# Performance work log

Measured on AMD Instinct MI355X. Metric: run time of the kernel, lower is better.

Reference implementation:

```python
import jax, jax.numpy as jnp
import numpy as np
from jax import lax

N = 100000   # n_nodes
E = 600000   # n_edges (no self loops by construction)
D = 128      # hidden_dim
L = 3        # n_hops
K = 5        # tail_k_threshold


def setup_inputs() -> dict:
    key = jax.random.key(0)
    ks = jax.random.split(key, 10)
    x = jax.random.normal(ks[0], (N, D), dtype=jnp.float32)
    src = jax.random.randint(ks[1], (E,), 0, N)
    off = jax.random.randint(ks[2], (E,), 1, N)
    dst = (src + off) % N  # guarantees dst != src (self loops removed in original)
    s = 1.0 / np.sqrt(D)
    def U(k, shape):
        return jax.random.uniform(k, shape, minval=-s, maxval=s, dtype=jnp.float32)
    return {
        "x": x,
        "G1": U(ks[3], (L, D, D)), "G2": U(ks[4], (L, D, D)),
        "B1": U(ks[5], (L, D, D)), "B2": U(ks[6], (L, D, D)),
        "R": U(ks[7], (L, D)),
        "edge_src": src, "edge_dst": dst,
    }


def _lrelu(v):
    return jax.nn.leaky_relu(v, 0.2)


def reference(x, G1, G2, B1, B2, R, edge_src, edge_dst):
    # row degrees of adj (A[src, dst] = 1)
    deg = jax.ops.segment_sum(jnp.ones(E, jnp.float32), edge_src, num_segments=N)
    inv_d = jnp.where(deg > 0, 1.0 / jnp.maximum(deg, 1.0), 0.0)   # left norm D^-1 A
    inv_d1 = 1.0 / (deg + 1.0)                                      # (A+I) left norm
    inv_d2 = 1.0 / (deg + 2.0)                                      # +1 virtual node
    w0, w1, w2 = inv_d[edge_src], inv_d1[edge_src], inv_d2[edge_src]
    head_mask = deg > K

    def spmm(w_edge, h):  # (D^-1 A) @ h via gather-scale-scatter
        return jax.ops.segment_sum(w_edge[:, None] * h[edge_dst], edge_src, num_segments=N)

    def propagate(head):
        h = x
        embs = [h]
        sups = []
        for l in range(L):
            nb = spmm(w0, h)
            ft = lax.stop_gradient(h)
            nbd = lax.stop_gradient(nb)
            gamma = _lrelu(ft @ G1[l].T + nbd @ G2[l].T) + 1.0
            beta = _lrelu(ft @ B1[l].T + nbd @ B2[l].T)
            m = ft + gamma * R[l] + beta - nbd   # missing_info (Relation, ablation=0)
            sups.append(m)
            if head:
                h = spmm(w1, h) + inv_d1[:, None] * h
            else:
                h = spmm(w2, h) + inv_d2[:, None] * h + m * inv_d2[:, None]
            embs.append(h)
        emb = jnp.mean(jnp.stack(embs, 0), 0)
        sup = jnp.mean(jnp.stack(sups, 0), 0)
        return emb, sup

    emb_h, _ = propagate(True)
    emb_t, _ = propagate(False)
    node_emb = jnp.where(head_mask[:, None], emb_h, emb_t)
    return node_emb
```

## Files before the change

### kernel.cpp

```cpp
#include <hip/hip_runtime.h>

#define N_NODES 100000
#define N_EDGES 600000
#define DIM 128
#define SCAN_B 1024
#define NCHUNK 98

typedef __attribute__((ext_vector_type(4))) float f32x4;
typedef __attribute__((ext_vector_type(8))) short bf16x8;
typedef __attribute__((ext_vector_type(4))) unsigned short u16x4;
typedef __attribute__((ext_vector_type(8))) unsigned short u16x8;

__device__ __forceinline__ unsigned short f2bf(float f) {
    union { float f; unsigned u; } cv; cv.f = f;
    unsigned r = (cv.u + 0x7FFFu + ((cv.u >> 16) & 1u)) >> 16;
    return (unsigned short)r;
}
__device__ __forceinline__ float bf2f(unsigned short v) {
    union { unsigned u; float f; } c; c.u = ((unsigned)v) << 16; return c.f;
}


__global__ void k_degree(const int* __restrict__ src, int* __restrict__ degi) {
    int e = blockIdx.x * 256 + threadIdx.x;
    if (e < N_EDGES) atomicAdd(&degi[src[e]], 1);
}

__global__ void k_chunksum(const int* __restrict__ degi, int* __restrict__ bsum) {
    __shared__ int sm[SCAN_B];
    int i = blockIdx.x * SCAN_B + threadIdx.x;
    sm[threadIdx.x] = (i < N_NODES) ? degi[i] : 0;
    __syncthreads();
    for (int s = SCAN_B / 2; s > 0; s >>= 1) {
        if (threadIdx.x < (unsigned)s) sm[threadIdx.x] += sm[threadIdx.x + s];
        __syncthreads();
    }
    if (threadIdx.x == 0) bsum[blockIdx.x] = sm[0];
}

__global__ void k_scanb(int* __restrict__ bsum, int nb) {
    __shared__ int sm[128];
    int t = threadIdx.x;
    int v = (t < nb) ? bsum[t] : 0;
    sm[t] = v; __syncthreads();
    for (int s = 1; s < 128; s <<= 1) {
        int a = (t >= s) ? sm[t - s] : 0;
        __syncthreads();
        sm[t] += a;
        __syncthreads();
    }
    if (t < nb) bsum[t] = sm[t] - v;
}

__global__ void k_rowptr(const int* __restrict__ degi, const int* __restrict__ bsum,
                         int* __restrict__ rowptr, int* __restrict__ cnt,
                         float* __restrict__ inv0, float* __restrict__ inv1,
                         float* __restrict__ inv2) {
    __shared__ int sm[SCAN_B];
    int i = blockIdx.x * SCAN_B + threadIdx.x;
    int v = (i < N_NODES) ? degi[i] : 0;
    sm[threadIdx.x] = v; __syncthreads();
    for (int s = 1; s < SCAN_B; s <<= 1) {
        int a = (threadIdx.x >= (unsigned)s) ? sm[threadIdx.x - s] : 0;
        __syncthreads();
        sm[threadIdx.x] += a;
        __syncthreads();
    }
    if (i < N_NODES) {
        int excl = bsum[blockIdx.x] + sm[threadIdx.x] - v;
        rowptr[i] = excl;
        cnt[i] = excl;
        float d = (float)v;
        inv0[i] = (v > 0) ? 1.0f / d : 0.0f;
        inv1[i] = 1.0f / (d + 1.0f);
        inv2[i] = 1.0f / (d + 2.0f);
    }
}

__global__ void k_fill(const int* __restrict__ src, const int* __restrict__ dst,
                       int* __restrict__ cnt, int* __restrict__ col) {
    int e = blockIdx.x * 256 + threadIdx.x;
    if (e < N_EDGES) {
        int pos = atomicAdd(&cnt[src[e]], 1);
        col[pos] = dst[e];
    }
}

__global__ void k_pack(const float* __restrict__ G1, const float* __restrict__ G2,
                       const float* __restrict__ B1, const float* __restrict__ B2,
                       short* __restrict__ Wp) {
    int idx = blockIdx.x * 256 + threadIdx.x;
    int j = idx & 7, lane = (idx >> 3) & 63, nt = (idx >> 9) & 15, kb = (idx >> 13) & 7, l = idx >> 16;
    int k = kb * 32 + (lane >> 4) * 8 + j;
    int n = nt * 16 + (lane & 15);
    float v;
    if (n < 128) {
        v = (k < 128) ? G1[(l * 128 + n) * 128 + k] : G2[(l * 128 + n) * 128 + (k - 128)];
    } else {
        int n2 = n - 128;
        v = (k < 128) ? B1[(l * 128 + n2) * 128 + k] : B2[(l * 128 + n2) * 128 + (k - 128)];
    }
    Wp[idx] = (short)f2bf(v);
}

__global__ void k_xcast(const float* __restrict__ x, unsigned short* __restrict__ xb) {
    int i = (blockIdx.x * 256 + threadIdx.x) * 4;
    f32x4 v = *(const f32x4*)(x + i);
    unsigned short o0 = f2bf(v[0]), o1 = f2bf(v[1]), o2 = f2bf(v[2]), o3 = f2bf(v[3]);
    unsigned long long pk = (unsigned long long)o0 | ((unsigned long long)o1 << 16)
                          | ((unsigned long long)o2 << 32) | ((unsigned long long)o3 << 48);
    *(unsigned long long*)(xb + i) = pk;
}


template <int NE>
__device__ __forceinline__ void gath_issue(const u16x8* __restrict__ h8,
        int idx, int base, int c, int d, float* acc) {
    u16x8 v[NE];
#pragma unroll
    for (int e = 0; e < NE; ++e) {
        int ce = __shfl(idx, base + e, 64);
        v[e] = h8[(size_t)ce * 16 + c];
    }
#pragma unroll
    for (int e = 0; e < NE; ++e) {
        if (e < d) {
#pragma unroll
            for (int j = 0; j < 8; ++j) acc[j] += bf2f(v[e][j]);
        }
    }
}

__device__ __forceinline__ void gather4(const u16x8* __restrict__ h8,
        const int* __restrict__ col, int start, int d, int lane, float* acc) {
    int c = lane & 15;
    int base = lane & 48;
    int dd = d < 16 ? d : 16;
    int idx = (c < dd) ? col[start + c] : 0;
    int dm = d;
    int tmx = __shfl_xor(dm, 16);
    dm = dm > tmx ? dm : tmx;
    tmx = __shfl_xor(dm, 32);
    dm = dm > tmx ? dm : tmx;
    if (dm <= 8) {
        gath_issue<8>(h8, idx, base, c, d, acc);
    } else {
        gath_issue<16>(h8, idx, base, c, d, acc);
        if (dm > 16) {
            for (int e = 16; e < d; ++e) {
                int c0 = col[start + e];
                u16x8 v = h8[(size_t)c0 * 16 + c];
#pragma unroll
                for (int j = 0; j < 8; ++j) acc[j] += bf2f(v[j]);
            }
        }
    }
}

template <int NE>
__device__ __forceinline__ void gath_issue2(const u16x8* __restrict__ hT,
        const u16x8* __restrict__ hH,
        int idx, int base, int c, int d, int e0, float* accT, float* accH) {
    u16x8 vT[NE], vH[NE];
#pragma unroll
    for (int e = 0; e < NE; ++e) {
        int ce = __shfl(idx, base + e0 + e, 64);
        vT[e] = hT[(size_t)ce * 16 + c];
        vH[e] = hH[(size_t)ce * 16 + c];
    }
#pragma unroll
    for (int e = 0; e < NE; ++e) {
        if (e0 + e < d) {
#pragma unroll
            for (int j = 0; j < 8; ++j) {
                accT[j] += bf2f(vT[e][j]);
                accH[j] += bf2f(vH[e][j]);
            }
        }
    }
}

__device__ __forceinline__ void gather4_dual(const u16x8* __restrict__ hT,
        const u16x8* __restrict__ hH,
        const int* __restrict__ col, int start, int d, int lane,
        float* accT, float* accH) {
    int c = lane & 15;
    int base = lane & 48;
    int dd = d < 16 ? d : 16;
    int idx = (c < dd) ? col[start + c] : 0;
    int dm = d;
    int tmx = __shfl_xor(dm, 16);
    dm = dm > tmx ? dm : tmx;
    tmx = __shfl_xor(dm, 32);
    dm = dm > tmx ? dm : tmx;
    if (dm <= 8) {
        gath_issue2<8>(hT, hH, idx, base, c, d, 0, accT, accH);
    } else {
        gath_issue2<8>(hT, hH, idx, base, c, d, 0, accT, accH);
        gath_issue2<8>(hT, hH, idx, base, c, d, 8, accT, accH);
        if (dm > 16) {
            for (int e = 16; e < d; ++e) {
                int c0 = col[start + e];
                u16x8 vT = hT[(size_t)c0 * 16 + c];
                u16x8 vH = hH[(size_t)c0 * 16 + c];
#pragma unroll
                for (int j = 0; j < 8; ++j) {
                    accT[j] += bf2f(vT[j]);
                    accH[j] += bf2f(vH[j]);
                }
            }
        }
    }
}

__device__ __forceinline__ void tail_gemm(
    int rb,
    unsigned short (*sH)[136], unsigned short (*sS)[136], unsigned short (*sO)[136],
    unsigned short* __restrict__ hb_next,
    const unsigned short* __restrict__ xb, const unsigned short* __restrict__ t1b,
    float* __restrict__ outp,
    const float* __restrict__ Rl, const short* __restrict__ Wp,
    const float* __restrict__ inv0, const float* __restrict__ inv2,
    const int* __restrict__ degi, int last)
{
    int wave = threadIdx.x >> 6, lane = threadIdx.x & 63;
    int q = lane >> 4, m = lane & 15;
    float w0 = inv0[rb + m];
    const short* wl = Wp + lane * 8;

    const f32x4 vz = {0.f, 0.f, 0.f, 0.f};
    f32x4 aA[2] = {vz, vz}, aB[2] = {vz, vz};

#pragma unroll
    for (int kb = 0; kb < 4; ++kb) {
        bf16x8 ah = *(const bf16x8*)&sH[m][kb * 32 + q * 8];
#pragma unroll
        for (int j = 0; j < 2; ++j) {
            bf16x8 b1v = *(const bf16x8*)(wl + (kb * 16 + 2 * wave + j) * 512);
            bf16x8 b2v = *(const bf16x8*)(wl + (kb * 16 + 2 * wave + 8 + j) * 512);
            aA[j] = __builtin_amdgcn_mfma_f32_16x16x32_bf16(ah, b1v, aA[j], 0, 0, 0);
            aB[j] = __builtin_amdgcn_mfma_f32_16x16x32_bf16(ah, b2v, aB[j], 0, 0, 0);
        }
    }
#pragma unroll
    for (int kb = 0; kb < 4; ++kb) {
        u16x8 sv = *(const u16x8*)&sS[m][kb * 32 + q * 8];
        bf16x8 as;
#pragma unroll
        for (int j = 0; j < 8; ++j) as[j] = (short)f2bf(w0 * bf2f(sv[j]));
#pragma unroll
        for (int j = 0; j < 2; ++j) {
            bf16x8 b1v = *(const bf16x8*)(wl + ((kb + 4) * 16 + 2 * wave + j) * 512);
            bf16x8 b2v = *(const bf16x8*)(wl + ((kb + 4) * 16 + 2 * wave + 8 + j) * 512);
            aA[j] = __builtin_amdgcn_mfma_f32_16x16x32_bf16(as, b1v, aA[j], 0, 0, 0);
            aB[j] = __builtin_amdgcn_mfma_f32_16x16x32_bf16(as, b2v, aB[j], 0, 0, 0);
        }
    }

    float Rv[2];
#pragma unroll
    for (int j = 0; j < 2; ++j) Rv[j] = Rl[(2 * wave + j) * 16 + m];

#pragma unroll
    for (int r = 0; r < 4; ++r) {
        int gi = rb + q * 4 + r;
        float wi0 = inv0[gi], wi2 = inv2[gi];
        int dgi = degi[gi];
#pragma unroll
        for (int j = 0; j < 2; ++j) {
            int cc = (2 * wave + j) * 16 + m;
            float z1 = aA[j][r], z2 = aB[j][r];
            float h = bf2f(sH[q * 4 + r][cc]);
            float sva = bf2f(sS[q * 4 + r][cc]);
            float ga = (z1 > 0.f ? z1 : 0.2f * z1) + 1.0f;
            float be = (z2 > 0.f ? z2 : 0.2f * z2);
            float mm = h + ga * Rv[j] + be - wi0 * sva;
            float hn = wi2 * (sva + h + mm);
            if (!last) {
                sO[q * 4 + r][cc] = f2bf(hn);
            } else if (dgi <= 5) {
                float xv = bf2f(xb[(size_t)gi * DIM + cc]);
                float t1 = bf2f(t1b[(size_t)gi * DIM + cc]);
                outp[(size_t)gi * DIM + cc] = 0.25f * (xv + t1 + h + hn);
            }
        }
    }
    if (!last) {
        __syncthreads();
        int g = lane >> 4, c = lane & 15;
        int row = rb + wave * 4 + g;
        ((u16x8*)hb_next)[(size_t)row * 16 + c] = *(u16x8*)&sO[wave * 4 + g][c * 8];
    }
}


__global__ __launch_bounds__(256, 4) void k_fused0(
    const unsigned short* __restrict__ xb, unsigned short* __restrict__ hA,
    unsigned short* __restrict__ tA, float* __restrict__ outp,
    const float* __restrict__ Rl, const short* __restrict__ Wp,
    const float* __restrict__ inv0, const float* __restrict__ inv1,
    const float* __restrict__ inv2,
    const int* __restrict__ rowptr, const int* __restrict__ degi,
    const int* __restrict__ col)
{
    __shared__ __align__(16) unsigned short sH[16][136], sS[16][136], sO[16][136];
    int rb = blockIdx.x * 16;
    int wave = threadIdx.x >> 6, lane = threadIdx.x & 63;
    {
        int g = lane >> 4, c = lane & 15;
        int row = rb + wave * 4 + g;
        int start = rowptr[row], d = degi[row];
        u16x8 hv = ((const u16x8*)xb)[(size_t)row * 16 + c];
        float acc[8] = {0,0,0,0,0,0,0,0};
        gather4((const u16x8*)xb, col, start, d, lane, acc);
        u16x8 so;
#pragma unroll
        for (int j = 0; j < 8; ++j) so[j] = f2bf(acc[j]);
        *(u16x8*)&sS[wave * 4 + g][c * 8] = so;
        *(u16x8*)&sH[wave * 4 + g][c * 8] = hv;
        float w1 = inv1[row];
        u16x8 ho;
#pragma unroll
        for (int j = 0; j < 8; ++j) ho[j] = f2bf(w1 * (acc[j] + bf2f(hv[j])));
        ((u16x8*)hA)[(size_t)row * 16 + c] = ho;
    }
    __syncthreads();
    tail_gemm(rb, sH, sS, sO, tA, xb, tA, outp, Rl, Wp, inv0, inv2, degi, 0);
}

__global__ __launch_bounds__(256, 4) void k_hop(
    const unsigned short* __restrict__ tb, unsigned short* __restrict__ tb_next,
    const unsigned short* __restrict__ hb, unsigned short* __restrict__ hb_next,
    const unsigned short* __restrict__ xb, const unsigned short* __restrict__ t1b,
    const unsigned short* __restrict__ h1b, float* __restrict__ outp,
    const float* __restrict__ Rl, const short* __restrict__ Wp,
    const float* __restrict__ inv0, const float* __restrict__ inv1,
    const float* __restrict__ inv2,
    const int* __restrict__ rowptr, const int* __restrict__ degi,
    const int* __restrict__ col, int last)
{
    __shared__ __align__(16) unsigned short sH[16][136], sS[16][136], sO[16][136];
    int rb = blockIdx.x * 16;
    int wave = threadIdx.x >> 6, lane = threadIdx.x & 63;

    {
        int g = lane >> 4, c = lane & 15;
        int row = rb + wave * 4 + g;
        int start = rowptr[row], d = degi[row];
        u16x8 tv = ((const u16x8*)tb)[(size_t)row * 16 + c];
        u16x8 hv = ((const u16x8*)hb)[(size_t)row * 16 + c];
        float accT[8] = {0,0,0,0,0,0,0,0};
        float accH[8] = {0,0,0,0,0,0,0,0};
        gather4_dual((const u16x8*)tb, (const u16x8*)hb, col, start, d, lane, accT, accH);

        u16x8 so;
#pragma unroll
        for (int j = 0; j < 8; ++j) so[j] = f2bf(accT[j]);
        *(u16x8*)&sS[wave * 4 + g][c * 8] = so;
        *(u16x8*)&sH[wave * 4 + g][c * 8] = tv;

        float w1 = inv1[row];
        if (!last) {
            u16x8 ho;
#pragma unroll
            for (int j = 0; j < 8; ++j) ho[j] = f2bf(w1 * (accH[j] + bf2f(hv[j])));
            ((u16x8*)hb_next)[(size_t)row * 16 + c] = ho;
        } else if (d > 5) {
            u16x8 xv = ((const u16x8*)xb)[(size_t)row * 16 + c];
            u16x8 h1 = ((const u16x8*)h1b)[(size_t)row * 16 + c];
            f32x4 e0, e1;
#pragma unroll
            for (int j = 0; j < 4; ++j) {
                float h2 = bf2f(hv[j]);
                e0[j] = 0.25f * (bf2f(xv[j]) + bf2f(h1[j]) + h2 + w1 * (accH[j] + h2));
            }
#pragma unroll
            for (int j = 0; j < 4; ++j) {
                float h2 = bf2f(hv[4 + j]);
                e1[j] = 0.25f * (bf2f(xv[4 + j]) + bf2f(h1[4 + j]) + h2 + w1 * (accH[4 + j] + h2));
            }
            float* op = outp + (size_t)row * DIM + c * 8;
            *(f32x4*)op = e0;
            *(f32x4*)(op + 4) = e1;
        }
    }
    __syncthreads();

    tail_gemm(rb, sH, sS, sO, tb_next, xb, t1b, outp, Rl, Wp, inv0, inv2, degi, last);
}


extern "C" void kernel_launch(void* const* d_in, const int* in_sizes, int n_in,
                              void* d_out, int out_size, void* d_ws, size_t ws_size,
                              hipStream_t stream) {
    const float* x  = (const float*)d_in[0];
    const float* G1 = (const float*)d_in[1];
    const float* G2 = (const float*)d_in[2];
    const float* B1 = (const float*)d_in[3];
    const float* B2 = (const float*)d_in[4];
    const float* R  = (const float*)d_in[5];
    const int* esrc = (const int*)d_in[6];
    const int* edst = (const int*)d_in[7];
    float* out = (float*)d_out;

    char* base = (char*)d_ws;
    size_t off = 0;
    auto alloc = [&](size_t b) -> void* {
        void* p = base + off;
        off = (off + b + 255) & ~(size_t)255;
        return p;
    };
    int* degi   = (int*)alloc(4 * N_NODES);
    int* rowptr = (int*)alloc(4 * N_NODES);
    int* cnt    = (int*)alloc(4 * N_NODES);
    int* bsum   = (int*)alloc(4 * 256);
    int* col    = (int*)alloc(4 * N_EDGES);
    float* inv0 = (float*)alloc(4 * N_NODES);
    float* inv1 = (float*)alloc(4 * N_NODES);
    float* inv2 = (float*)alloc(4 * N_NODES);
    short* Wp   = (short*)alloc(2 * 3 * 65536);
    unsigned short* xb = (unsigned short*)alloc(2ull * N_NODES * DIM);
    unsigned short* hA = (unsigned short*)alloc(2ull * N_NODES * DIM);
    unsigned short* hB = (unsigned short*)alloc(2ull * N_NODES * DIM);
    unsigned short* tA = (unsigned short*)alloc(2ull * N_NODES * DIM);
    unsigned short* tB = (unsigned short*)alloc(2ull * N_NODES * DIM);

    hipMemsetAsync(degi, 0, 4 * N_NODES, stream);
    k_degree<<<(N_EDGES + 255) / 256, 256, 0, stream>>>(esrc, degi);
    k_chunksum<<<NCHUNK, SCAN_B, 0, stream>>>(degi, bsum);
    k_scanb<<<1, 128, 0, stream>>>(bsum, NCHUNK);
    k_rowptr<<<NCHUNK, SCAN_B, 0, stream>>>(degi, bsum, rowptr, cnt, inv0, inv1, inv2);
    k_fill<<<(N_EDGES + 255) / 256, 256, 0, stream>>>(esrc, edst, cnt, col);
    k_pack<<<768, 256, 0, stream>>>(G1, G2, B1, B2, Wp);
    k_xcast<<<12500, 256, 0, stream>>>(x, xb);

    k_fused0<<<6250, 256, 0, stream>>>(xb, hA, tA, out, R, Wp,
                                       inv0, inv1, inv2, rowptr, degi, col);

    k_hop<<<6250, 256, 0, stream>>>(tA, tB, hA, hB, xb, tA, hA, out,
                                    R + 128, Wp + 65536,
                                    inv0, inv1, inv2, rowptr, degi, col, 0);

    k_hop<<<6250, 256, 0, stream>>>(tB, (unsigned short*)0, hB, (unsigned short*)0,
                                    xb, tA, hA, out,
                                    R + 256, Wp + 131072,
                                    inv0, inv1, inv2, rowptr, degi, col, 1);
}
```

Measured before the change: 397.2 us.

## Interleave tail and head states per node and process 32 rows per block

Replaces the separate tail and head bf16 buffers with one interleaved buffer per hop, so each node's t and h rows sit next to each other (256 halves per node). A neighbour gather then reads one contiguous 512-byte span instead of two scattered 256-byte reads. Blocks now cover 32 rows instead of 16, which reuses the weight fragments across two MFMA row tiles and halves the grid. The cost is more LDS and register use per block, which may lower occupancy.

```diff
diff --git a/kernel.cpp b/kernel.cpp
--- a/kernel.cpp
+++ b/kernel.cpp
@@ -158,15 +158,15 @@
 }
 
 template <int NE>
-__device__ __forceinline__ void gath_issue2(const u16x8* __restrict__ hT,
-        const u16x8* __restrict__ hH,
+__device__ __forceinline__ void gath_issue2c(const u16x8* __restrict__ st8,
         int idx, int base, int c, int d, int e0, float* accT, float* accH) {
     u16x8 vT[NE], vH[NE];
 #pragma unroll
     for (int e = 0; e < NE; ++e) {
         int ce = __shfl(idx, base + e0 + e, 64);
-        vT[e] = hT[(size_t)ce * 16 + c];
-        vH[e] = hH[(size_t)ce * 16 + c];
+        size_t b = (size_t)ce * 32 + c;
+        vT[e] = st8[b];
+        vH[e] = st8[b + 16];
     }
 #pragma unroll
     for (int e = 0; e < NE; ++e) {
@@ -180,8 +180,7 @@
     }
 }
 
-__device__ __forceinline__ void gather4_dual(const u16x8* __restrict__ hT,
-        const u16x8* __restrict__ hH,
+__device__ __forceinline__ void gather4_dualc(const u16x8* __restrict__ st8,
         const int* __restrict__ col, int start, int d, int lane,
         float* accT, float* accH) {
     int c = lane & 15;
@@ -194,15 +193,16 @@
     tmx = __shfl_xor(dm, 32);
     dm = dm > tmx ? dm : tmx;
     if (dm <= 8) {
-        gath_issue2<8>(hT, hH, idx, base, c, d, 0, accT, accH);
+        gath_issue2c<8>(st8, idx, base, c, d, 0, accT, accH);
     } else {
-        gath_issue2<8>(hT, hH, idx, base, c, d, 0, accT, accH);
-        gath_issue2<8>(hT, hH, idx, base, c, d, 8, accT, accH);
+        gath_issue2c<8>(st8, idx, base, c, d, 0, accT, accH);
+        gath_issue2c<8>(st8, idx, base, c, d, 8, accT, accH);
         if (dm > 16) {
             for (int e = 16; e < d; ++e) {
                 int c0 = col[start + e];
-                u16x8 vT = hT[(size_t)c0 * 16 + c];
-                u16x8 vH = hH[(size_t)c0 * 16 + c];
+                size_t b = (size_t)c0 * 32 + c;
+                u16x8 vT = st8[b];
+                u16x8 vH = st8[b + 16];
 #pragma unroll
                 for (int j = 0; j < 8; ++j) {
                     accT[j] += bf2f(vT[j]);
@@ -213,11 +213,12 @@
     }
 }
 
-__device__ __forceinline__ void tail_gemm(
+__device__ __forceinline__ void tail_gemm32(
     int rb,
     unsigned short (*sH)[136], unsigned short (*sS)[136], unsigned short (*sO)[136],
-    unsigned short* __restrict__ hb_next,
-    const unsigned short* __restrict__ xb, const unsigned short* __restrict__ t1b,
+    unsigned short* __restrict__ stn,
+    const unsigned short* __restrict__ st1,
+    const unsigned short* __restrict__ xb,
     float* __restrict__ outp,
     const float* __restrict__ Rl, const short* __restrict__ Wp,
     const float* __restrict__ inv0, const float* __restrict__ inv2,
@@ -225,35 +226,44 @@
 {
     int wave = threadIdx.x >> 6, lane = threadIdx.x & 63;
     int q = lane >> 4, m = lane & 15;
-    float w0 = inv0[rb + m];
+    float w0a = inv0[rb + m], w0b = inv0[rb + 16 + m];
     const short* wl = Wp + lane * 8;
 
     const f32x4 vz = {0.f, 0.f, 0.f, 0.f};
-    f32x4 aA[2] = {vz, vz}, aB[2] = {vz, vz};
+    f32x4 aA[2][2] = {{vz, vz}, {vz, vz}}, aB[2][2] = {{vz, vz}, {vz, vz}};
 
 #pragma unroll
     for (int kb = 0; kb < 4; ++kb) {
-        bf16x8 ah = *(const bf16x8*)&sH[m][kb * 32 + q * 8];
+        bf16x8 ah0 = *(const bf16x8*)&sH[m][kb * 32 + q * 8];
+        bf16x8 ah1 = *(const bf16x8*)&sH[16 + m][kb * 32 + q * 8];
 #pragma unroll
         for (int j = 0; j < 2; ++j) {
             bf16x8 b1v = *(const bf16x8*)(wl + (kb * 16 + 2 * wave + j) * 512);
             bf16x8 b2v = *(const bf16x8*)(wl + (kb * 16 + 2 * wave + 8 + j) * 512);
-            aA[j] = __builtin_amdgcn_mfma_f32_16x16x32_bf16(ah, b1v, aA[j], 0, 0, 0);
-            aB[j] = __builtin_amdgcn_mfma_f32_16x16x32_bf16(ah, b2v, aB[j], 0, 0, 0);
+            aA[0][j] = __builtin_amdgcn_mfma_f32_16x16x32_bf16(ah0, b1v, aA[0][j], 0, 0, 0);
+            aA[1][j] = __builtin_amdgcn_mfma_f32_16x16x32_bf16(ah1, b1v, aA[1][j], 0, 0, 0);
+            aB[0][j] = __builtin_amdgcn_mfma_f32_16x16x32_bf16(ah0, b2v, aB[0][j], 0, 0, 0);
+            aB[1][j] = __builtin_amdgcn_mfma_f32_16x16x32_bf16(ah1, b2v, aB[1][j], 0, 0, 0);
         }
     }
 #pragma unroll
     for (int kb = 0; kb < 4; ++kb) {
-        u16x8 sv = *(const u16x8*)&sS[m][kb * 32 + q * 8];
-        bf16x8 as;
-#pragma unroll
-        for (int j = 0; j < 8; ++j) as[j] = (short)f2bf(w0 * bf2f(sv[j]));
+        u16x8 sv0 = *(const u16x8*)&sS[m][kb * 32 + q * 8];
+        u16x8 sv1 = *(const u16x8*)&sS[16 + m][kb * 32 + q * 8];
+        bf16x8 as0, as1;
+#pragma unroll
+        for (int j = 0; j < 8; ++j) {
+            as0[j] = (short)f2bf(w0a * bf2f(sv0[j]));
+            as1[j] = (short)f2bf(w0b * bf2f(sv1[j]));
+        }
 #pragma unroll
         for (int j = 0; j < 2; ++j) {
             bf16x8 b1v = *(const bf16x8*)(wl + ((kb + 4) * 16 + 2 * wave + j) * 512);
             bf16x8 b2v = *(const bf16x8*)(wl + ((kb + 4) * 16 + 2 * wave + 8 + j) * 512);
-            aA[j] = __builtin_amdgcn_mfma_f32_16x16x32_bf16(as, b1v, aA[j], 0, 0, 0);
-            aB[j] = __builtin_amdgcn_mfma_f32_16x16x32_bf16(as, b2v, aB[j], 0, 0, 0);
+            aA[0][j] = __builtin_amdgcn_mfma_f32_16x16x32_bf16(as0, b1v, aA[0][j], 0, 0, 0);
+            aA[1][j] = __builtin_amdgcn_mfma_f32_16x16x32_bf16(as1, b1v, aA[1][j], 0, 0, 0);
+            aB[0][j] = __builtin_amdgcn_mfma_f32_16x16x32_bf16(as0, b2v, aB[0][j], 0, 0, 0);
+            aB[1][j] = __builtin_amdgcn_mfma_f32_16x16x32_bf16(as1, b2v, aB[1][j], 0, 0, 0);
         }
     }
 
@@ -262,112 +272,123 @@
     for (int j = 0; j < 2; ++j) Rv[j] = Rl[(2 * wave + j) * 16 + m];
 
 #pragma unroll
-    for (int r = 0; r < 4; ++r) {
-        int gi = rb + q * 4 + r;
-        float wi0 = inv0[gi], wi2 = inv2[gi];
-        int dgi = degi[gi];
-#pragma unroll
-        for (int j = 0; j < 2; ++j) {
-            int cc = (2 * wave + j) * 16 + m;
-            float z1 = aA[j][r], z2 = aB[j][r];
-            float h = bf2f(sH[q * 4 + r][cc]);
-            float sva = bf2f(sS[q * 4 + r][cc]);
-            float ga = (z1 > 0.f ? z1 : 0.2f * z1) + 1.0f;
-            float be = (z2 > 0.f ? z2 : 0.2f * z2);
-            float mm = h + ga * Rv[j] + be - wi0 * sva;
-            float hn = wi2 * (sva + h + mm);
-            if (!last) {
-                sO[q * 4 + r][cc] = f2bf(hn);
-            } else if (dgi <= 5) {
-                float xv = bf2f(xb[(size_t)gi * DIM + cc]);
-                float t1 = bf2f(t1b[(size_t)gi * DIM + cc]);
-                outp[(size_t)gi * DIM + cc] = 0.25f * (xv + t1 + h + hn);
+    for (int t = 0; t < 2; ++t) {
+#pragma unroll
+        for (int r = 0; r < 4; ++r) {
+            int rl = t * 16 + q * 4 + r;
+            int gi = rb + rl;
+            float wi0 = inv0[gi], wi2 = inv2[gi];
+            int dgi = degi[gi];
+#pragma unroll
+            for (int j = 0; j < 2; ++j) {
+                int cc = (2 * wave + j) * 16 + m;
+                float z1 = aA[t][j][r], z2 = aB[t][j][r];
+                float h = bf2f(sH[rl][cc]);
+                float sva = bf2f(sS[rl][cc]);
+                float ga = (z1 > 0.f ? z1 : 0.2f * z1) + 1.0f;
+                float be = (z2 > 0.f ? z2 : 0.2f * z2);
+                float mm = h + ga * Rv[j] + be - wi0 * sva;
+                float hn = wi2 * (sva + h + mm);
+                if (!last) {
+                    sO[rl][cc] = f2bf(hn);
+                } else if (dgi <= 5) {
+                    float xv = bf2f(xb[(size_t)gi * DIM + cc]);
+                    float t1 = bf2f(st1[(size_t)gi * 256 + cc]);
+                    outp[(size_t)gi * DIM + cc] = 0.25f * (xv + t1 + h + hn);
+                }
             }
         }
     }
     if (!last) {
         __syncthreads();
         int g = lane >> 4, c = lane & 15;
-        int row = rb + wave * 4 + g;
-        ((u16x8*)hb_next)[(size_t)row * 16 + c] = *(u16x8*)&sO[wave * 4 + g][c * 8];
+#pragma unroll
+        for (int it = 0; it < 2; ++it) {
+            int rl = wave * 8 + it * 4 + g;
+            ((u16x8*)stn)[(size_t)(rb + rl) * 32 + c] = *(u16x8*)&sO[rl][c * 8];
+        }
     }
 }
 
 
 __global__ __launch_bounds__(256, 4) void k_fused0(
-    const unsigned short* __restrict__ xb, unsigned short* __restrict__ hA,
-    unsigned short* __restrict__ tA, float* __restrict__ outp,
+    const unsigned short* __restrict__ xb, unsigned short* __restrict__ st1,
     const float* __restrict__ Rl, const short* __restrict__ Wp,
     const float* __restrict__ inv0, const float* __restrict__ inv1,
     const float* __restrict__ inv2,
     const int* __restrict__ rowptr, const int* __restrict__ degi,
     const int* __restrict__ col)
 {
-    __shared__ __align__(16) unsigned short sH[16][136], sS[16][136], sO[16][136];
-    int rb = blockIdx.x * 16;
+    __shared__ __align__(16) unsigned short sH[32][136], sS[32][136], sO[32][136];
+    int rb = blockIdx.x * 32;
     int wave = threadIdx.x >> 6, lane = threadIdx.x & 63;
-    {
-        int g = lane >> 4, c = lane & 15;
-        int row = rb + wave * 4 + g;
+    int g = lane >> 4, c = lane & 15;
+#pragma unroll
+    for (int it = 0; it < 2; ++it) {
+        int rl = wave * 8 + it * 4 + g;
+        int row = rb + rl;
         int start = rowptr[row], d = degi[row];
-        u16x8 hv = ((const u16x8*)xb)[(size_t)row * 16 + c];
+        u16x8 xv = ((const u16x8*)xb)[(size_t)row * 16 + c];
         float acc[8] = {0,0,0,0,0,0,0,0};
         gather4((const u16x8*)xb, col, start, d, lane, acc);
         u16x8 so;
 #pragma unroll
         for (int j = 0; j < 8; ++j) so[j] = f2bf(acc[j]);
-        *(u16x8*)&sS[wave * 4 + g][c * 8] = so;
-        *(u16x8*)&sH[wave * 4 + g][c * 8] = hv;
+        *(u16x8*)&sS[rl][c * 8] = so;
+        *(u16x8*)&sH[rl][c * 8] = xv;
         float w1 = inv1[row];
         u16x8 ho;
 #pragma unroll
-        for (int j = 0; j < 8; ++j) ho[j] = f2bf(w1 * (acc[j] + bf2f(hv[j])));
-        ((u16x8*)hA)[(size_t)row * 16 + c] = ho;
+        for (int j = 0; j < 8; ++j) ho[j] = f2bf(w1 * (acc[j] + bf2f(xv[j])));
+        ((u16x8*)st1)[(size_t)row * 32 + 16 + c] = ho;
     }
     __syncthreads();
-    tail_gemm(rb, sH, sS, sO, tA, xb, tA, outp, Rl, Wp, inv0, inv2, degi, 0);
+    tail_gemm32(rb, sH, sS, sO, st1, st1, xb, (float*)0,
+                Rl, Wp, inv0, inv2, degi, 0);
 }
 
 __global__ __launch_bounds__(256, 4) void k_hop(
-    const unsigned short* __restrict__ tb, unsigned short* __restrict__ tb_next,
-    const unsigned short* __restrict__ hb, unsigned short* __restrict__ hb_next,
-    const unsigned short* __restrict__ xb, const unsigned short* __restrict__ t1b,
-    const unsigned short* __restrict__ h1b, float* __restrict__ outp,
+    const unsigned short* __restrict__ st, unsigned short* __restrict__ stn,
+    const unsigned short* __restrict__ st1,
+    const unsigned short* __restrict__ xb, float* __restrict__ outp,
     const float* __restrict__ Rl, const short* __restrict__ Wp,
     const float* __restrict__ inv0, const float* __restrict__ inv1,
     const float* __restrict__ inv2,
     const int* __restrict__ rowptr, const int* __restrict__ degi,
     const int* __restrict__ col, int last)
 {
-    __shared__ __align__(16) unsigned short sH[16][136], sS[16][136], sO[16][136];
-    int rb = blockIdx.x * 16;
+    __shared__ __align__(16) unsigned short sH[32][136], sS[32][136], sO[32][136];
+    int rb = blockIdx.x * 32;
     int wave = threadIdx.x >> 6, lane = threadIdx.x & 63;
-
-    {
-        int g = lane >> 4, c = lane & 15;
-        int row = rb + wave * 4 + g;
+    int g = lane >> 4, c = lane & 15;
+
+#pragma unroll
+    for (int it = 0; it < 2; ++it) {
+        int rl = wave * 8 + it * 4 + g;
+        int row = rb + rl;
         int start = rowptr[row], d = degi[row];
-        u16x8 tv = ((const u16x8*)tb)[(size_t)row * 16 + c];
-        u16x8 hv = ((const u16x8*)hb)[(size_t)row * 16 + c];
+        size_t ro = (size_t)row * 32 + c;
+        u16x8 tv = ((const u16x8*)st)[ro];
+        u16x8 hv = ((const u16x8*)st)[ro + 16];
         float accT[8] = {0,0,0,0,0,0,0,0};
         float accH[8] = {0,0,0,0,0,0,0,0};
-        gather4_dual((const u16x8*)tb, (const u16x8*)hb, col, start, d, lane, accT, accH);
+        gather4_dualc((const u16x8*)st, col, start, d, lane, accT, accH);
 
         u16x8 so;
 #pragma unroll
         for (int j = 0; j < 8; ++j) so[j] = f2bf(accT[j]);
-        *(u16x8*)&sS[wave * 4 + g][c * 8] = so;
-        *(u16x8*)&sH[wave * 4 + g][c * 8] = tv;
+        *(u16x8*)&sS[rl][c * 8] = so;
+        *(u16x8*)&sH[rl][c * 8] = tv;
 
         float w1 = inv1[row];
         if (!last) {
             u16x8 ho;
 #pragma unroll
             for (int j = 0; j < 8; ++j) ho[j] = f2bf(w1 * (accH[j] + bf2f(hv[j])));
-            ((u16x8*)hb_next)[(size_t)row * 16 + c] = ho;
+            ((u16x8*)stn)[ro + 16] = ho;
         } else if (d > 5) {
             u16x8 xv = ((const u16x8*)xb)[(size_t)row * 16 + c];
-            u16x8 h1 = ((const u16x8*)h1b)[(size_t)row * 16 + c];
+            u16x8 h1 = ((const u16x8*)st1)[(size_t)row * 32 + 16 + c];
             f32x4 e0, e1;
 #pragma unroll
             for (int j = 0; j < 4; ++j) {
@@ -386,7 +407,8 @@
     }
     __syncthreads();
 
-    tail_gemm(rb, sH, sS, sO, tb_next, xb, t1b, outp, Rl, Wp, inv0, inv2, degi, last);
+    tail_gemm32(rb, sH, sS, sO, stn, st1, xb, outp,
+                Rl, Wp, inv0, inv2, degi, last);
 }
 
 
@@ -419,11 +441,9 @@
     float* inv1 = (float*)alloc(4 * N_NODES);
     float* inv2 = (float*)alloc(4 * N_NODES);
     short* Wp   = (short*)alloc(2 * 3 * 65536);
-    unsigned short* xb = (unsigned short*)alloc(2ull * N_NODES * DIM);
-    unsigned short* hA = (unsigned short*)alloc(2ull * N_NODES * DIM);
-    unsigned short* hB = (unsigned short*)alloc(2ull * N_NODES * DIM);
-    unsigned short* tA = (unsigned short*)alloc(2ull * N_NODES * DIM);
-    unsigned short* tB = (unsigned short*)alloc(2ull * N_NODES * DIM);
+    unsigned short* xb  = (unsigned short*)alloc(2ull * N_NODES * DIM);
+    unsigned short* st1 = (unsigned short*)alloc(4ull * N_NODES * DIM);
+    unsigned short* st2 = (unsigned short*)alloc(4ull * N_NODES * DIM);
 
     hipMemsetAsync(degi, 0, 4 * N_NODES, stream);
     k_degree<<<(N_EDGES + 255) / 256, 256, 0, stream>>>(esrc, degi);
@@ -434,15 +454,14 @@
     k_pack<<<768, 256, 0, stream>>>(G1, G2, B1, B2, Wp);
     k_xcast<<<12500, 256, 0, stream>>>(x, xb);
 
-    k_fused0<<<6250, 256, 0, stream>>>(xb, hA, tA, out, R, Wp,
+    k_fused0<<<3125, 256, 0, stream>>>(xb, st1, R, Wp,
                                        inv0, inv1, inv2, rowptr, degi, col);
 
-    k_hop<<<6250, 256, 0, stream>>>(tA, tB, hA, hB, xb, tA, hA, out,
+    k_hop<<<3125, 256, 0, stream>>>(st1, st2, st1, xb, out,
                                     R + 128, Wp + 65536,
                                     inv0, inv1, inv2, rowptr, degi, col, 0);
 
-    k_hop<<<6250, 256, 0, stream>>>(tB, (unsigned short*)0, hB, (unsigned short*)0,
-                                    xb, tA, hA, out,
+    k_hop<<<3125, 256, 0, stream>>>(st2, (unsigned short*)0, st1, xb, out,
                                     R + 256, Wp + 131072,
                                     inv0, inv1, inv2, rowptr, degi, col, 1);
 }
```

New measurement: 397.5 us. About the same (+0.1%).
